# Kernel tuning notes

Measured on AMD Instinct MI355X. Metric: run time of the kernel, lower is better.

The kernel has to match this reference:

```python
import jax, jax.numpy as jnp
import numpy as np

WIN = 7            # skimage default win_size
K1 = 0.01
K2 = 0.03
DATA_RANGE = 1.0   # images are in [0, 1]
PAD = (WIN - 1) // 2


def _uniform_filter_valid(x):
    # x: [N, 1, H, W] -> valid 7x7 box filter (== skimage uniform_filter cropped by PAD)
    k = jnp.ones((1, 1, WIN, WIN), x.dtype) / (WIN * WIN)
    return jax.lax.conv_general_dilated(
        x, k, window_strides=(1, 1), padding='VALID',
        dimension_numbers=('NCHW', 'OIHW', 'NCHW'))


def _ssim_mean(a, b):
    # a, b: [B, C, H, W]; each [H, W] slice is one independent SSIM image
    B, C, H, W = a.shape
    x = a.reshape(B * C, 1, H, W)
    y = b.reshape(B * C, 1, H, W)

    ux = _uniform_filter_valid(x)
    uy = _uniform_filter_valid(y)
    uxx = _uniform_filter_valid(x * x)
    uyy = _uniform_filter_valid(y * y)
    uxy = _uniform_filter_valid(x * y)

    NP = WIN * WIN
    cov_norm = NP / (NP - 1.0)  # sample covariance correction (skimage default)
    vx = cov_norm * (uxx - ux * ux)
    vy = cov_norm * (uyy - uy * uy)
    vxy = cov_norm * (uxy - ux * uy)

    C1 = (K1 * DATA_RANGE) ** 2
    C2 = (K2 * DATA_RANGE) ** 2

    S = ((2.0 * ux * uy + C1) * (2.0 * vxy + C2)) / \
        ((ux * ux + uy * uy + C1) * (vx + vy + C2))

    # skimage crops PAD border then means; VALID conv already cropped it.
    # All images are the same size, so np.average(per-image means) == global mean.
    return jnp.mean(S)


def setup_inputs() -> dict:
    key = jax.random.key(0)
    k1, k2 = jax.random.split(key)
    pred = jax.random.uniform(k1, (32, 4, 384, 384), dtype=jnp.float32)
    actual = jax.random.uniform(k2, (32, 4, 384, 384), dtype=jnp.float32)
    return {"pred": pred, "actual": actual}


def reference(pred, actual):
    return _ssim_mean(pred, actual)
```

## Files before the change

kernel.cpp:

```cpp
#include <hip/hip_runtime.h>

#define WIN 7
#define OUT_W 126
#define OUT_H 15
#define IN_W 132
#define IN_H 21
#define PITCH 132
#define AELEM (OUT_H * PITCH)
#define H 384
#define W 384
#define OH 378
#define OW 378
#define NIMG 128
#define TX 3
#define TY 26
#define NBLK (TX * TY * NIMG)

__device__ __forceinline__ float wave_reduce(float v) {
#pragma unroll
    for (int off = 32; off > 0; off >>= 1) v += __shfl_down(v, off, 64);
    return v;
}

__global__ __launch_bounds__(256, 5) void ssim_main(const float* __restrict__ pred,
                                                    const float* __restrict__ act,
                                                    float* __restrict__ partials) {
    __shared__ __align__(16) float cs[4 * AELEM + 16];
    __shared__ float red[4];

    const int t = threadIdx.x;
    const int x0 = blockIdx.x * OUT_W;
    const int y0 = blockIdx.y * OUT_H;
    const size_t base = (size_t)blockIdx.z * H * W;

    if (t < IN_W) {
        const int col = x0 + t;
        const float* xc = pred + base + col;
        const float* yc = act + base + col;
        float xv[IN_H], yv[IN_H];
#pragma unroll
        for (int i = 0; i < IN_H; ++i) {
            const int row = y0 + i;
            const bool ok = row < H;
            xv[i] = ok ? xc[(size_t)row * W] : 0.f;
            yv[i] = ok ? yc[(size_t)row * W] : 0.f;
        }
        float sx = 0.f, sy = 0.f, sq = 0.f, sxy = 0.f;
#pragma unroll
        for (int k = 0; k < WIN; ++k) {
            sx += xv[k];
            sy += yv[k];
            sq = fmaf(xv[k], xv[k], fmaf(yv[k], yv[k], sq));
            sxy = fmaf(xv[k], yv[k], sxy);
        }
        cs[0 * AELEM + t] = sx;
        cs[1 * AELEM + t] = sy;
        cs[2 * AELEM + t] = sq;
        cs[3 * AELEM + t] = sxy;
#pragma unroll
        for (int r = 1; r < OUT_H; ++r) {
            const float xn = xv[r + 6], yn = yv[r + 6];
            const float xo = xv[r - 1], yo = yv[r - 1];
            sx += xn - xo;
            sy += yn - yo;
            sq = fmaf(xn, xn, fmaf(yn, yn, fmaf(-xo, xo, fmaf(-yo, yo, sq))));
            sxy = fmaf(xn, yn, fmaf(-xo, yo, sxy));
            const int a = r * PITCH + t;
            cs[0 * AELEM + a] = sx;
            cs[1 * AELEM + a] = sy;
            cs[2 * AELEM + a] = sq;
            cs[3 * AELEM + a] = sxy;
        }
    }
    __syncthreads();

    const int r = t & 15;
    const int g = t >> 4;
    const int c0 = g * 8;

    const float C1B = 0.2401f;
    const float C2B = 2.1168f;

    float acc = 0.f;
    if (r < OUT_H && (y0 + r) < OH) {
        float S[4][8];
#pragma unroll
        for (int a = 0; a < 4; ++a) {
            const float* bp = &cs[a * AELEM + r * PITCH + c0];
            const float4 q0 = *(const float4*)(bp);
            const float4 q1 = *(const float4*)(bp + 4);
            const float4 q2 = *(const float4*)(bp + 8);
            const float4 q3 = *(const float4*)(bp + 12);
            const float v[16] = {q0.x, q0.y, q0.z, q0.w, q1.x, q1.y, q1.z, q1.w,
                                 q2.x, q2.y, q2.z, q2.w, q3.x, q3.y, q3.z, q3.w};
            float s = ((v[0] + v[1]) + (v[2] + v[3])) + ((v[4] + v[5]) + v[6]);
            S[a][0] = s;
#pragma unroll
            for (int j = 1; j < 8; ++j) {
                s += v[j + 6] - v[j - 1];
                S[a][j] = s;
            }
        }
        const int nmax = OUT_W - c0;
#pragma unroll
        for (int j = 0; j < 8; ++j) {
            const float Sx = S[0][j], Sy = S[1][j];
            const float Sq = S[2][j], Sxy = S[3][j];
            const float p = Sx * Sy;
            const float qq = fmaf(Sx, Sx, Sy * Sy);
            const float n1 = fmaf(2.f, p, C1B);
            const float n2 = fmaf(98.f, Sxy, fmaf(-2.f, p, C2B));
            const float d1 = qq + C1B;
            const float d2 = fmaf(49.f, Sq, C2B - qq);
            const float s = (n1 * n2) * __builtin_amdgcn_rcpf(d1 * d2);
            acc = (j < nmax) ? acc + s : acc;
        }
    }

    const float wsum = wave_reduce(acc);
    if ((t & 63) == 0) red[t >> 6] = wsum;
    __syncthreads();
    if (t == 0) {
        partials[blockIdx.x + TX * (blockIdx.y + TY * blockIdx.z)] =
            red[0] + red[1] + red[2] + red[3];
    }
}

__global__ __launch_bounds__(1024) void ssim_finalize(const float* __restrict__ partials,
                                                      float* __restrict__ out) {
    __shared__ double red[1024];
    const int t = threadIdx.x;
    double s = 0.0;
    for (int i = t; i < NBLK; i += 1024) s += (double)partials[i];
    red[t] = s;
    __syncthreads();
#pragma unroll
    for (int off = 512; off > 0; off >>= 1) {
        if (t < off) red[t] += red[t + off];
        __syncthreads();
    }
    if (t == 0) out[0] = (float)(red[0] / ((double)NIMG * OH * OW));
}

extern "C" void kernel_launch(void* const* d_in, const int* in_sizes, int n_in,
                              void* d_out, int out_size, void* d_ws, size_t ws_size,
                              hipStream_t stream) {
    const float* pred = (const float*)d_in[0];
    const float* act  = (const float*)d_in[1];
    float* partials = (float*)d_ws;
    dim3 grid(TX, TY, NIMG);
    ssim_main<<<grid, 256, 0, stream>>>(pred, act, partials);
    ssim_finalize<<<1, 1024, 0, stream>>>(partials, (float*)d_out);
}
```

Measured before the change: 166.2 us.

## Switch to full-width row strips with rolling vertical sums in chunks of seven

Replaces the 2D tiling (126x15 output tiles with halo reloads) with full-width blocks of 384 threads that each walk a 49-row strip, keeping a 7-row ring of inputs in registers and writing vertical sums into shared memory in 7-row chunks. This removes the horizontal halo and most of the vertical halo re-reads, and keeps the running sums across chunks. The shared layout also changes to interleaved float2 planes so each horizontal pass loads pairs with float4 reads. In exchange there are two barriers per chunk and fewer blocks (1024), with only 336 of 384 threads doing the horizontal pass, so latency hiding may suffer.

```diff
diff --git a/kernel.cpp b/kernel.cpp
--- a/kernel.cpp
+++ b/kernel.cpp
@@ -1,20 +1,18 @@
 #include <hip/hip_runtime.h>
 
-#define WIN 7
-#define OUT_W 126
-#define OUT_H 15
-#define IN_W 132
-#define IN_H 21
-#define PITCH 132
-#define AELEM (OUT_H * PITCH)
+
 #define H 384
 #define W 384
-#define OH 378
-#define OW 378
+#define OWIDTH 378
 #define NIMG 128
-#define TX 3
-#define TY 26
-#define NBLK (TX * TY * NIMG)
+#define CH 7
+#define P2 394
+#define PLANE (CH * P2)
+#define SY 49
+#define NSTRIP 8
+#define NBLK (NSTRIP * NIMG)
+#define NGRP 48
+#define NSLOT (NGRP * CH)
 
 __device__ __forceinline__ float wave_reduce(float v) {
 #pragma unroll
@@ -22,98 +20,139 @@
     return v;
 }
 
-__global__ __launch_bounds__(256, 5) void ssim_main(const float* __restrict__ pred,
+#define VSTEP(SLOT, LR, XN, YN) do {                                      \
+    const float xo = xv[SLOT], yo = yv[SLOT];                             \
+    const float xn = (XN), yn = (YN);                                     \
+    sx += xn - xo; sy += yn - yo;                                         \
+    sq = fmaf(xn, xn, fmaf(yn, yn, fmaf(-xo, xo, fmaf(-yo, yo, sq))));    \
+    sxy = fmaf(xn, yn, fmaf(-xo, yo, sxy));                               \
+    xv[SLOT] = xn; yv[SLOT] = yn;                                         \
+    stA[(LR) * P2 + t] = make_float2(sx, sy);                             \
+    stB[(LR) * P2 + t] = make_float2(sq, sxy);                            \
+} while (0)
+
+__global__ __launch_bounds__(384, 5) void ssim_main(const float* __restrict__ pred,
                                                     const float* __restrict__ act,
                                                     float* __restrict__ partials) {
-    __shared__ __align__(16) float cs[4 * AELEM + 16];
-    __shared__ float red[4];
+    __shared__ __align__(16) float2 st[2 * PLANE];
+    __shared__ float red[6];
 
     const int t = threadIdx.x;
-    const int x0 = blockIdx.x * OUT_W;
-    const int y0 = blockIdx.y * OUT_H;
-    const size_t base = (size_t)blockIdx.z * H * W;
+    const int y0 = blockIdx.x * SY;
+    const int nrows = (blockIdx.x == NSTRIP - 1) ? (OWIDTH - (NSTRIP - 1) * SY) : SY;
+    const int nch = nrows / CH;
+    const size_t base = (size_t)blockIdx.y * (H * W);
 
-    if (t < IN_W) {
-        const int col = x0 + t;
-        const float* xc = pred + base + col;
-        const float* yc = act + base + col;
-        float xv[IN_H], yv[IN_H];
-#pragma unroll
-        for (int i = 0; i < IN_H; ++i) {
-            const int row = y0 + i;
-            const bool ok = row < H;
-            xv[i] = ok ? xc[(size_t)row * W] : 0.f;
-            yv[i] = ok ? yc[(size_t)row * W] : 0.f;
-        }
-        float sx = 0.f, sy = 0.f, sq = 0.f, sxy = 0.f;
-#pragma unroll
-        for (int k = 0; k < WIN; ++k) {
-            sx += xv[k];
-            sy += yv[k];
-            sq = fmaf(xv[k], xv[k], fmaf(yv[k], yv[k], sq));
-            sxy = fmaf(xv[k], yv[k], sxy);
-        }
-        cs[0 * AELEM + t] = sx;
-        cs[1 * AELEM + t] = sy;
-        cs[2 * AELEM + t] = sq;
-        cs[3 * AELEM + t] = sxy;
-#pragma unroll
-        for (int r = 1; r < OUT_H; ++r) {
-            const float xn = xv[r + 6], yn = yv[r + 6];
-            const float xo = xv[r - 1], yo = yv[r - 1];
-            sx += xn - xo;
-            sy += yn - yo;
-            sq = fmaf(xn, xn, fmaf(yn, yn, fmaf(-xo, xo, fmaf(-yo, yo, sq))));
-            sxy = fmaf(xn, yn, fmaf(-xo, yo, sxy));
-            const int a = r * PITCH + t;
-            cs[0 * AELEM + a] = sx;
-            cs[1 * AELEM + a] = sy;
-            cs[2 * AELEM + a] = sq;
-            cs[3 * AELEM + a] = sxy;
-        }
-    }
-    __syncthreads();
+    float2* const stA = st;
+    float2* const stB = st + PLANE;
 
-    const int r = t & 15;
-    const int g = t >> 4;
+    const float* xp = pred + base + (size_t)y0 * W + t;
+    const float* ap = act  + base + (size_t)y0 * W + t;
+
+    const int g = t / 7;
+    const int r = t - 7 * g;
     const int c0 = g * 8;
-
+    const int nmax = OWIDTH - c0;
     const float C1B = 0.2401f;
     const float C2B = 2.1168f;
+    float acc = 0.f;
 
-    float acc = 0.f;
-    if (r < OUT_H && (y0 + r) < OH) {
-        float S[4][8];
+    float xv[7], yv[7];
+    float sx = 0.f, sy = 0.f, sq = 0.f, sxy = 0.f;
 #pragma unroll
-        for (int a = 0; a < 4; ++a) {
-            const float* bp = &cs[a * AELEM + r * PITCH + c0];
-            const float4 q0 = *(const float4*)(bp);
-            const float4 q1 = *(const float4*)(bp + 4);
-            const float4 q2 = *(const float4*)(bp + 8);
-            const float4 q3 = *(const float4*)(bp + 12);
-            const float v[16] = {q0.x, q0.y, q0.z, q0.w, q1.x, q1.y, q1.z, q1.w,
-                                 q2.x, q2.y, q2.z, q2.w, q3.x, q3.y, q3.z, q3.w};
-            float s = ((v[0] + v[1]) + (v[2] + v[3])) + ((v[4] + v[5]) + v[6]);
-            S[a][0] = s;
+    for (int i = 0; i < 7; ++i) {
+        xv[i] = xp[i * W];
+        yv[i] = ap[i * W];
+    }
+#pragma unroll
+    for (int i = 0; i < 7; ++i) {
+        sx += xv[i]; sy += yv[i];
+        sq = fmaf(xv[i], xv[i], fmaf(yv[i], yv[i], sq));
+        sxy = fmaf(xv[i], yv[i], sxy);
+    }
+    stA[t] = make_float2(sx, sy);
+    stB[t] = make_float2(sq, sxy);
+    {
+        float nx[6], ny[6];
+#pragma unroll
+        for (int i = 0; i < 6; ++i) {
+            nx[i] = xp[(7 + i) * W];
+            ny[i] = ap[(7 + i) * W];
+        }
+#pragma unroll
+        for (int i = 1; i < 7; ++i) VSTEP(i - 1, i, nx[i - 1], ny[i - 1]);
+    }
+
+    int c = 0;
+    while (true) {
+        __syncthreads();
+        if (t < NSLOT) {
+            const float4* qa = (const float4*)(stA + r * P2 + c0);
+            float4 a[8];
+#pragma unroll
+            for (int k = 0; k < 8; ++k) a[k] = qa[k];
+            float vx[16], vy[16];
+#pragma unroll
+            for (int k = 0; k < 8; ++k) {
+                vx[2 * k]     = a[k].x; vy[2 * k]     = a[k].y;
+                vx[2 * k + 1] = a[k].z; vy[2 * k + 1] = a[k].w;
+            }
+            float S0[8], S1[8];
+            float sA = ((vx[0] + vx[1]) + (vx[2] + vx[3])) + ((vx[4] + vx[5]) + vx[6]);
+            float sB = ((vy[0] + vy[1]) + (vy[2] + vy[3])) + ((vy[4] + vy[5]) + vy[6]);
+            S0[0] = sA; S1[0] = sB;
 #pragma unroll
             for (int j = 1; j < 8; ++j) {
-                s += v[j + 6] - v[j - 1];
-                S[a][j] = s;
+                sA += vx[j + 6] - vx[j - 1]; S0[j] = sA;
+                sB += vy[j + 6] - vy[j - 1]; S1[j] = sB;
+            }
+            const float4* qb = (const float4*)(stB + r * P2 + c0);
+            float4 b[8];
+#pragma unroll
+            for (int k = 0; k < 8; ++k) b[k] = qb[k];
+            float vq[16], vw[16];
+#pragma unroll
+            for (int k = 0; k < 8; ++k) {
+                vq[2 * k]     = b[k].x; vw[2 * k]     = b[k].y;
+                vq[2 * k + 1] = b[k].z; vw[2 * k + 1] = b[k].w;
+            }
+            float s2 = ((vq[0] + vq[1]) + (vq[2] + vq[3])) + ((vq[4] + vq[5]) + vq[6]);
+            float s3 = ((vw[0] + vw[1]) + (vw[2] + vw[3])) + ((vw[4] + vw[5]) + vw[6]);
+#pragma unroll
+            for (int j = 0; j < 8; ++j) {
+                if (j) {
+                    s2 += vq[j + 6] - vq[j - 1];
+                    s3 += vw[j + 6] - vw[j - 1];
+                }
+                const float Sx = S0[j], Sy = S1[j];
+                const float Sq = s2, Sxy = s3;
+                const float p  = Sx * Sy;
+                const float qq = fmaf(Sx, Sx, Sy * Sy);
+                const float n1 = fmaf(2.f, p, C1B);
+                const float n2 = fmaf(98.f, Sxy, fmaf(-2.f, p, C2B));
+                const float d1 = qq + C1B;
+                const float d2 = fmaf(49.f, Sq, C2B - qq);
+                const float s  = (n1 * n2) * __builtin_amdgcn_rcpf(d1 * d2);
+                acc = (j < nmax) ? acc + s : acc;
             }
         }
-        const int nmax = OUT_W - c0;
+        if (++c == nch) break;
+        __syncthreads();
+        {
+            const int rb = 7 * c + 6;
+            float nx[7], ny[7];
 #pragma unroll
-        for (int j = 0; j < 8; ++j) {
-            const float Sx = S[0][j], Sy = S[1][j];
-            const float Sq = S[2][j], Sxy = S[3][j];
-            const float p = Sx * Sy;
-            const float qq = fmaf(Sx, Sx, Sy * Sy);
-            const float n1 = fmaf(2.f, p, C1B);
-            const float n2 = fmaf(98.f, Sxy, fmaf(-2.f, p, C2B));
-            const float d1 = qq + C1B;
-            const float d2 = fmaf(49.f, Sq, C2B - qq);
-            const float s = (n1 * n2) * __builtin_amdgcn_rcpf(d1 * d2);
-            acc = (j < nmax) ? acc + s : acc;
+            for (int i = 0; i < 7; ++i) {
+                nx[i] = xp[(rb + i) * W];
+                ny[i] = ap[(rb + i) * W];
+            }
+            VSTEP(6, 0, nx[0], ny[0]);
+            VSTEP(0, 1, nx[1], ny[1]);
+            VSTEP(1, 2, nx[2], ny[2]);
+            VSTEP(2, 3, nx[3], ny[3]);
+            VSTEP(3, 4, nx[4], ny[4]);
+            VSTEP(4, 5, nx[5], ny[5]);
+            VSTEP(5, 6, nx[6], ny[6]);
         }
     }
 
@@ -121,8 +160,8 @@
     if ((t & 63) == 0) red[t >> 6] = wsum;
     __syncthreads();
     if (t == 0) {
-        partials[blockIdx.x + TX * (blockIdx.y + TY * blockIdx.z)] =
-            red[0] + red[1] + red[2] + red[3];
+        partials[blockIdx.x + NSTRIP * blockIdx.y] =
+            ((red[0] + red[1]) + (red[2] + red[3])) + (red[4] + red[5]);
     }
 }
 
@@ -139,7 +178,7 @@
         if (t < off) red[t] += red[t + off];
         __syncthreads();
     }
-    if (t == 0) out[0] = (float)(red[0] / ((double)NIMG * OH * OW));
+    if (t == 0) out[0] = (float)(red[0] / ((double)NIMG * OWIDTH * OWIDTH));
 }
 
 extern "C" void kernel_launch(void* const* d_in, const int* in_sizes, int n_in,
@@ -148,7 +187,7 @@
     const float* pred = (const float*)d_in[0];
     const float* act  = (const float*)d_in[1];
     float* partials = (float*)d_ws;
-    dim3 grid(TX, TY, NIMG);
-    ssim_main<<<grid, 256, 0, stream>>>(pred, act, partials);
+    dim3 grid(NSTRIP, NIMG);
+    ssim_main<<<grid, 384, 0, stream>>>(pred, act, partials);
     ssim_finalize<<<1, 1024, 0, stream>>>(partials, (float*)d_out);
 }
```

New measurement: 178.7 us. 7.5% more time.

## Use single-wave blocks streaming row strips with ring-buffered column sums

Applied to the files above, without the earlier changes.

Replaces the 256-thread tile kernel with one-wavefront blocks that each cover a 58-column by 64-row strip. Column sums are packed as float4 in an 8-row LDS ring buffer, and global loads for the next 8 rows are issued before the current rows' SSIM is computed, so memory latency overlaps compute. Block-level syncs go away in favour of wave-level waitcnt and sched barriers. The aim is to cut halo re-reads and barrier stalls and to keep loads in flight, at the cost of more registers and a grid of small blocks.

```diff
diff --git a/kernel.cpp b/kernel.cpp
--- a/kernel.cpp
+++ b/kernel.cpp
@@ -1,20 +1,17 @@
 #include <hip/hip_runtime.h>
 
-#define WIN 7
-#define OUT_W 126
-#define OUT_H 15
-#define IN_W 132
-#define IN_H 21
-#define PITCH 132
-#define AELEM (OUT_H * PITCH)
+
 #define H 384
 #define W 384
-#define OH 378
-#define OW 378
+#define IMGSZ (H * W)
+#define OWIDTH 378
 #define NIMG 128
-#define TX 3
-#define TY 26
-#define NBLK (TX * TY * NIMG)
+#define NCT 7
+#define NRS 6
+#define WPI (NCT * NRS)
+#define NBLK (NIMG * WPI)
+#define P4 65
+#define CH 8
 
 __device__ __forceinline__ float wave_reduce(float v) {
 #pragma unroll
@@ -22,108 +19,122 @@
     return v;
 }
 
-__global__ __launch_bounds__(256, 5) void ssim_main(const float* __restrict__ pred,
-                                                    const float* __restrict__ act,
-                                                    float* __restrict__ partials) {
-    __shared__ __align__(16) float cs[4 * AELEM + 16];
-    __shared__ float red[4];
+#define VST(SN, SO, LR, XN, YN) do {                                      \
+    const float xo = xv[SO], yo = yv[SO];                                 \
+    const float xn = (XN), yn = (YN);                                     \
+    sx += xn - xo; sy += yn - yo;                                         \
+    sq = fmaf(xn, xn, fmaf(yn, yn, fmaf(-xo, xo, fmaf(-yo, yo, sq))));    \
+    sxy = fmaf(xn, yn, fmaf(-xo, yo, sxy));                               \
+    xv[SN] = xn; yv[SN] = yn;                                             \
+    st[(LR) * P4 + t] = make_float4(sx, sy, sq, sxy);                     \
+} while (0)
+
+__global__ __launch_bounds__(64, 4) void ssim_main(const float* __restrict__ pred,
+                                                   const float* __restrict__ act,
+                                                   float* __restrict__ partials) {
+    __shared__ __align__(16) float4 st[CH * P4 + 5];
 
     const int t = threadIdx.x;
-    const int x0 = blockIdx.x * OUT_W;
-    const int y0 = blockIdx.y * OUT_H;
-    const size_t base = (size_t)blockIdx.z * H * W;
+    const int wid = blockIdx.x;
+    const int img = wid / WPI;
+    const int rem = wid - img * WPI;
+    const int rs = rem / NCT;
+    const int ct = rem - rs * NCT;
 
-    if (t < IN_W) {
-        const int col = x0 + t;
-        const float* xc = pred + base + col;
-        const float* yc = act + base + col;
-        float xv[IN_H], yv[IN_H];
+    const int c0 = ct * 58;
+    const bool last_rs = (rs == NRS - 1);
+    const int y0 = last_rs ? (H - 70) : rs * 64;
+    const int ylo = last_rs ? 6 : 0;
+    const int nc_raw = OWIDTH - c0;
+    const int ncols = (nc_raw < 58) ? nc_raw : 58;
+
+    int col = c0 + t;
+    col = (col < W) ? col : (W - 1);
+    const float* px = pred + (size_t)img * IMGSZ + (size_t)y0 * W + col;
+    const float* py = act  + (size_t)img * IMGSZ + (size_t)y0 * W + col;
+
+    float xv[8], yv[8];
+    float pfx[7], pfy[7];
 #pragma unroll
-        for (int i = 0; i < IN_H; ++i) {
-            const int row = y0 + i;
-            const bool ok = row < H;
-            xv[i] = ok ? xc[(size_t)row * W] : 0.f;
-            yv[i] = ok ? yc[(size_t)row * W] : 0.f;
-        }
-        float sx = 0.f, sy = 0.f, sq = 0.f, sxy = 0.f;
+    for (int i = 0; i < 7; ++i) { xv[i] = px[i * W]; yv[i] = py[i * W]; }
 #pragma unroll
-        for (int k = 0; k < WIN; ++k) {
-            sx += xv[k];
-            sy += yv[k];
-            sq = fmaf(xv[k], xv[k], fmaf(yv[k], yv[k], sq));
-            sxy = fmaf(xv[k], yv[k], sxy);
-        }
-        cs[0 * AELEM + t] = sx;
-        cs[1 * AELEM + t] = sy;
-        cs[2 * AELEM + t] = sq;
-        cs[3 * AELEM + t] = sxy;
+    for (int i = 0; i < 7; ++i) { pfx[i] = px[(7 + i) * W]; pfy[i] = py[(7 + i) * W]; }
+    float sx = 0.f, sy = 0.f, sq = 0.f, sxy = 0.f;
 #pragma unroll
-        for (int r = 1; r < OUT_H; ++r) {
-            const float xn = xv[r + 6], yn = yv[r + 6];
-            const float xo = xv[r - 1], yo = yv[r - 1];
-            sx += xn - xo;
-            sy += yn - yo;
-            sq = fmaf(xn, xn, fmaf(yn, yn, fmaf(-xo, xo, fmaf(-yo, yo, sq))));
-            sxy = fmaf(xn, yn, fmaf(-xo, yo, sxy));
-            const int a = r * PITCH + t;
-            cs[0 * AELEM + a] = sx;
-            cs[1 * AELEM + a] = sy;
-            cs[2 * AELEM + a] = sq;
-            cs[3 * AELEM + a] = sxy;
-        }
+    for (int i = 0; i < 7; ++i) {
+        sx += xv[i]; sy += yv[i];
+        sq = fmaf(xv[i], xv[i], fmaf(yv[i], yv[i], sq));
+        sxy = fmaf(xv[i], yv[i], sxy);
     }
-    __syncthreads();
+    st[t] = make_float4(sx, sy, sq, sxy);
+    VST(7, 0, 1, pfx[0], pfy[0]);
+    VST(0, 1, 2, pfx[1], pfy[1]);
+    VST(1, 2, 3, pfx[2], pfy[2]);
+    VST(2, 3, 4, pfx[3], pfy[3]);
+    VST(3, 4, 5, pfx[4], pfy[4]);
+    VST(4, 5, 6, pfx[5], pfy[5]);
+    VST(5, 6, 7, pfx[6], pfy[6]);
 
-    const int r = t & 15;
-    const int g = t >> 4;
-    const int c0 = g * 8;
-
+    const int r = t >> 3;
+    const int k = t & 7;
+    const int nmax = ncols - 8 * k;
+    const float4* qbase = st + r * P4 + 8 * k;
     const float C1B = 0.2401f;
     const float C2B = 2.1168f;
+    float acc = 0.f;
 
-    float acc = 0.f;
-    if (r < OUT_H && (y0 + r) < OH) {
-        float S[4][8];
+    for (int c = 0; c < 8; ++c) {
+        float nfx[8], nfy[8];
+        if (c < 7) {
 #pragma unroll
-        for (int a = 0; a < 4; ++a) {
-            const float* bp = &cs[a * AELEM + r * PITCH + c0];
-            const float4 q0 = *(const float4*)(bp);
-            const float4 q1 = *(const float4*)(bp + 4);
-            const float4 q2 = *(const float4*)(bp + 8);
-            const float4 q3 = *(const float4*)(bp + 12);
-            const float v[16] = {q0.x, q0.y, q0.z, q0.w, q1.x, q1.y, q1.z, q1.w,
-                                 q2.x, q2.y, q2.z, q2.w, q3.x, q3.y, q3.z, q3.w};
-            float s = ((v[0] + v[1]) + (v[2] + v[3])) + ((v[4] + v[5]) + v[6]);
-            S[a][0] = s;
-#pragma unroll
-            for (int j = 1; j < 8; ++j) {
-                s += v[j + 6] - v[j - 1];
-                S[a][j] = s;
+            for (int i = 0; i < 8; ++i) {
+                nfx[i] = px[(8 * c + 14 + i) * W];
+                nfy[i] = py[(8 * c + 14 + i) * W];
             }
         }
-        const int nmax = OUT_W - c0;
+        float4 q[14];
+#pragma unroll
+        for (int j = 0; j < 14; ++j) q[j] = qbase[j];
+        float Sx  = ((q[0].x + q[1].x) + (q[2].x + q[3].x)) + ((q[4].x + q[5].x) + q[6].x);
+        float Sy  = ((q[0].y + q[1].y) + (q[2].y + q[3].y)) + ((q[4].y + q[5].y) + q[6].y);
+        float Sq  = ((q[0].z + q[1].z) + (q[2].z + q[3].z)) + ((q[4].z + q[5].z) + q[6].z);
+        float Sxy = ((q[0].w + q[1].w) + (q[2].w + q[3].w)) + ((q[4].w + q[5].w) + q[6].w);
+        const bool rowok = (8 * c + r) >= ylo;
 #pragma unroll
         for (int j = 0; j < 8; ++j) {
-            const float Sx = S[0][j], Sy = S[1][j];
-            const float Sq = S[2][j], Sxy = S[3][j];
-            const float p = Sx * Sy;
+            if (j) {
+                Sx  += q[j + 6].x - q[j - 1].x;
+                Sy  += q[j + 6].y - q[j - 1].y;
+                Sq  += q[j + 6].z - q[j - 1].z;
+                Sxy += q[j + 6].w - q[j - 1].w;
+            }
+            const float p  = Sx * Sy;
             const float qq = fmaf(Sx, Sx, Sy * Sy);
             const float n1 = fmaf(2.f, p, C1B);
             const float n2 = fmaf(98.f, Sxy, fmaf(-2.f, p, C2B));
             const float d1 = qq + C1B;
             const float d2 = fmaf(49.f, Sq, C2B - qq);
-            const float s = (n1 * n2) * __builtin_amdgcn_rcpf(d1 * d2);
-            acc = (j < nmax) ? acc + s : acc;
+            const float s  = (n1 * n2) * __builtin_amdgcn_rcpf(d1 * d2);
+            acc = (rowok && (j < nmax)) ? acc + s : acc;
+        }
+        __builtin_amdgcn_sched_barrier(0);
+        asm volatile("s_waitcnt lgkmcnt(0)" ::: "memory");
+        __builtin_amdgcn_sched_barrier(0);
+        if (c < 7) {
+            VST(6, 7, 0, nfx[0], nfy[0]);
+            VST(7, 0, 1, nfx[1], nfy[1]);
+            VST(0, 1, 2, nfx[2], nfy[2]);
+            VST(1, 2, 3, nfx[3], nfy[3]);
+            VST(2, 3, 4, nfx[4], nfy[4]);
+            VST(3, 4, 5, nfx[5], nfy[5]);
+            VST(4, 5, 6, nfx[6], nfy[6]);
+            VST(5, 6, 7, nfx[7], nfy[7]);
+            __builtin_amdgcn_sched_barrier(0);
         }
     }
 
     const float wsum = wave_reduce(acc);
-    if ((t & 63) == 0) red[t >> 6] = wsum;
-    __syncthreads();
-    if (t == 0) {
-        partials[blockIdx.x + TX * (blockIdx.y + TY * blockIdx.z)] =
-            red[0] + red[1] + red[2] + red[3];
-    }
+    if (t == 0) partials[wid] = wsum;
 }
 
 __global__ __launch_bounds__(1024) void ssim_finalize(const float* __restrict__ partials,
@@ -139,7 +150,7 @@
         if (t < off) red[t] += red[t + off];
         __syncthreads();
     }
-    if (t == 0) out[0] = (float)(red[0] / ((double)NIMG * OH * OW));
+    if (t == 0) out[0] = (float)(red[0] / ((double)NIMG * OWIDTH * OWIDTH));
 }
 
 extern "C" void kernel_launch(void* const* d_in, const int* in_sizes, int n_in,
@@ -148,7 +159,6 @@
     const float* pred = (const float*)d_in[0];
     const float* act  = (const float*)d_in[1];
     float* partials = (float*)d_ws;
-    dim3 grid(TX, TY, NIMG);
-    ssim_main<<<grid, 256, 0, stream>>>(pred, act, partials);
+    ssim_main<<<NBLK, 64, 0, stream>>>(pred, act, partials);
     ssim_finalize<<<1, 1024, 0, stream>>>(partials, (float*)d_out);
 }
```

Result: slower. 172.7 us (+3.9%).
